# Optimization experiments

Measured on AMD Instinct MI355X. Metric: run time of the kernel, lower is better.

The kernel has to match this reference:

```python
import jax, jax.numpy as jnp
import numpy as np

B, N_HEADS, F_TOK = 8, 12, 768
GRID_H, GRID_W = 32, 32
N_TOK = 1 + GRID_H * GRID_W  # 1025 (readout token + patches)
F_HEAD = F_TOK // N_HEADS    # 64
NUM_DIST = (2 * GRID_H - 1) * (2 * GRID_W - 1) + 3  # 3972


def _build_relpos_index(gh, gw):
    # BEiT-style relative position index with 3 extra slots for the readout token
    coords = np.stack(np.meshgrid(np.arange(gh), np.arange(gw), indexing='ij'))  # (2, gh, gw)
    flat = coords.reshape(2, -1)                                                 # (2, gh*gw)
    rel = flat[:, :, None] - flat[:, None, :]                                    # (2, P, P)
    rel = rel.transpose(1, 2, 0).astype(np.int64)                                # (P, P, 2)
    rel[:, :, 0] += gh - 1
    rel[:, :, 1] += gw - 1
    rel[:, :, 0] *= 2 * gw - 1
    rpi = rel.sum(-1)                                                            # (P, P)
    n = 1 + gh * gw
    nd = (2 * gh - 1) * (2 * gw - 1) + 3
    idx = np.zeros((n, n), dtype=np.int32)
    idx[1:, 1:] = rpi
    idx[0, :] = nd - 3  # readout -> all
    idx[:, 0] = nd - 2  # all -> readout
    idx[0, 0] = nd - 1  # readout -> readout
    return idx


def setup_inputs() -> dict:
    key = jax.random.key(0)
    ks = jax.random.split(key, 7)
    tokens = jax.random.normal(ks[0], (B, N_TOK, F_TOK), dtype=jnp.float32)
    qkv_w = jax.random.normal(ks[1], (3 * F_TOK, F_TOK), dtype=jnp.float32) * 0.02
    q_bias = jax.random.normal(ks[2], (1, N_HEADS, 1, F_HEAD), dtype=jnp.float32) * 0.02
    v_bias = jax.random.normal(ks[3], (1, N_HEADS, 1, F_HEAD), dtype=jnp.float32) * 0.02
    relpos_table = jax.random.normal(ks[4], (NUM_DIST, N_HEADS), dtype=jnp.float32) * 0.02
    proj_w = jax.random.normal(ks[5], (F_TOK, F_TOK), dtype=jnp.float32) * 0.02
    proj_b = jax.random.normal(ks[6], (F_TOK,), dtype=jnp.float32) * 0.02
    relpos_index = jnp.asarray(_build_relpos_index(GRID_H, GRID_W))  # (N, N) int32
    return {
        'tokens': tokens, 'qkv_w': qkv_w, 'q_bias': q_bias, 'v_bias': v_bias,
        'relpos_table': relpos_table, 'proj_w': proj_w, 'proj_b': proj_b,
        'relpos_index': relpos_index, 'patch_h': GRID_H, 'patch_w': GRID_W,
    }


def reference(tokens, qkv_w, q_bias, v_bias, relpos_table, proj_w, proj_b,
              relpos_index, patch_h, patch_w):
    b, n, f_tok = tokens.shape
    # qkv projection (no bias): (B, N, 3F) -> (3, B, H, N, f)
    qkv = tokens @ qkv_w.T
    qkv = qkv.reshape(b, n, 3, N_HEADS, F_HEAD).transpose(2, 0, 3, 1, 4)
    q, k, v = qkv[0], qkv[1], qkv[2]
    q = (q + q_bias) * (F_HEAD ** -0.5)
    v = v + v_bias
    # attention scores: (B, H, N, N)
    attn = jnp.einsum('bhnf,bhmf->bhnm', q, k)
    # relative position bias gather: (N, N, H) -> (H, N, N)
    bias = relpos_table[relpos_index].transpose(2, 0, 1)
    attn = attn + bias[None]
    w = jax.nn.softmax(attn, axis=-1)
    out = jnp.einsum('bhnm,bhmf->bhnf', w, v)
    out = out.transpose(0, 2, 1, 3).reshape(b, n, N_HEADS * F_HEAD)
    return out @ proj_w.T + proj_b
```

## Files before the change

kernel.cpp:

```cpp
#include <hip/hip_runtime.h>

#define B_ 8
#define NH 12
#define NTOK 1025
#define FT 768
#define MROWS (B_*NTOK)
#define NPAD2 1088
#define CH2 34
#define NQT 36
#define NTT 34
#define NRT18 18
#define LOG2E 1.44269504089f

typedef __bf16 bf16x8 __attribute__((ext_vector_type(8)));
typedef __bf16 bf16x2 __attribute__((ext_vector_type(2)));
typedef float floatx4 __attribute__((ext_vector_type(4)));
typedef float floatx16 __attribute__((ext_vector_type(16)));
typedef int intx4 __attribute__((ext_vector_type(4)));

__device__ __forceinline__ void async_ld16(const void* gp, void* lp) {
  __builtin_amdgcn_global_load_lds(
      (const __attribute__((address_space(1))) void*)gp,
      (__attribute__((address_space(3))) void*)lp, 16, 0, 0);
}

__global__ __launch_bounds__(256) void cvt_bf16(const float* __restrict__ src,
                                                __bf16* __restrict__ dst, int n4) {
  int i = blockIdx.x * 256 + threadIdx.x;
  if (i >= n4) return;
  float4 v = ((const float4*)src)[i];
  __bf16 o[4] = {(__bf16)v.x, (__bf16)v.y, (__bf16)v.z, (__bf16)v.w};
  *(uint2*)(dst + 4 * (size_t)i) = *(uint2*)o;
}

__global__ __launch_bounds__(256) void bias_gather_t(
    const int* __restrict__ idx, const float* __restrict__ table,
    __bf16* __restrict__ Bb) {
  const int qt = blockIdx.x, tt = blockIdx.y;
  const int t = threadIdx.x;
  const int lane = t & 63, w = t >> 6;
  const int l31 = lane & 31, hb = lane >> 5;
  int qrow = qt * 32 + l31; if (qrow > NTOK - 1) qrow = NTOK - 1;
  int ids[16]; bool ok[16];
#pragma unroll
  for (int j = 0; j < 16; ++j) {
    const int token = tt * 32 + (j & 3) + 8 * (j >> 2) + 4 * hb;
    ok[j] = token < NTOK;
    ids[j] = ok[j] ? idx[qrow * NTOK + token] : 0;
  }
#pragma unroll
  for (int g = 0; g < 3; ++g) {
    const int h = w + g * 4;
    __bf16 v[16];
#pragma unroll
    for (int j = 0; j < 16; ++j)
      v[j] = ok[j] ? (__bf16)(table[ids[j] * NH + h] * LOG2E) : (__bf16)(-1e30f);
    uint4* dst = (uint4*)(Bb + (((size_t)h * NQT + qt) * NTT + tt) * 1024 + lane * 16);
    dst[0] = ((uint4*)v)[0];
    dst[1] = ((uint4*)v)[1];
  }
}

__device__ __forceinline__ void gemm128_pipe(
    const __bf16* __restrict__ A, const __bf16* __restrict__ W,
    int m0, int n0, int M, __bf16* At, __bf16* Bt, floatx4 acc[4][4]) {
  const int tid = threadIdx.x, wave = tid >> 6, lane = tid & 63;
  const int l = lane & 15, qd = lane >> 4;
  const int wr = wave >> 1, wc = wave & 1;
  const int srow = lane >> 2, sg = lane & 3;
  const int r0 = wave * 32 + srow, r1 = r0 + 16;
  int gm0 = m0 + r0; if (gm0 >= M) gm0 = M - 1;
  int gm1 = m0 + r1; if (gm1 >= M) gm1 = M - 1;
  const int sw0 = (sg ^ (r0 & 3)) * 8;
  const __bf16* gA0 = A + (size_t)gm0 * FT + sw0;
  const __bf16* gA1 = A + (size_t)gm1 * FT + sw0;
  const __bf16* gB0 = W + (size_t)(n0 + r0) * FT + sw0;
  const __bf16* gB1 = W + (size_t)(n0 + r1) * FT + sw0;
  const int woff = wave * 32 * 32;
  const int fsw = (qd ^ (l & 3)) * 8;

  auto issue = [&](int k, int buf) {
    __bf16* a = At + buf * 4096 + woff;
    __bf16* b = Bt + buf * 4096 + woff;
    async_ld16(gA0 + k * 32, a);
    async_ld16(gA1 + k * 32, a + 512);
    async_ld16(gB0 + k * 32, b);
    async_ld16(gB1 + k * 32, b + 512);
  };
  auto step = [&](int buf) {
    __builtin_amdgcn_s_barrier();
    const __bf16* ab = At + buf * 4096;
    const __bf16* bb = Bt + buf * 4096;
    bf16x8 aF[4], bF[4];
#pragma unroll
    for (int t = 0; t < 4; ++t)
      aF[t] = *(const bf16x8*)(ab + (wr * 64 + t * 16 + l) * 32 + fsw);
#pragma unroll
    for (int u = 0; u < 4; ++u)
      bF[u] = *(const bf16x8*)(bb + (wc * 64 + u * 16 + l) * 32 + fsw);
#pragma unroll
    for (int t = 0; t < 4; ++t)
#pragma unroll
      for (int u = 0; u < 4; ++u)
        acc[t][u] = __builtin_amdgcn_mfma_f32_16x16x32_bf16(aF[t], bF[u], acc[t][u], 0, 0, 0);
  };

  issue(0, 0);
  int bk = 0;
  for (int k = 0; k < 23; ++k) {
    int bn = bk + 1; if (bn == 3) bn = 0;
    issue(k + 1, bn);
    __builtin_amdgcn_s_waitcnt(0x0F74);
    step(bk);
    bk = bn;
  }
  __builtin_amdgcn_s_waitcnt(0x0F70);
  step(bk);
}

__global__ __launch_bounds__(256) void qkv_gemm128(
    const __bf16* __restrict__ tokens, const __bf16* __restrict__ qkvw,
    const float* __restrict__ qbias, const float* __restrict__ vbias,
    __bf16* __restrict__ Qb, __bf16* __restrict__ Kc, __bf16* __restrict__ Vc) {
  __shared__ __bf16 At[3 * 4096], Bt[3 * 4096];
  const int u0 = blockIdx.x;
  const int c = u0 & 7, q0 = u0 >> 3;
  const int mi = (q0 / 18) * 8 + c, ni = q0 % 18;
  if (mi >= 65) return;
  const int m0 = mi * 128, n0 = ni * 128;
  const int tid = threadIdx.x, wave = tid >> 6, lane = tid & 63;
  const int l = lane & 15, qd = lane >> 4;
  const int wr = wave >> 1, wc = wave & 1;
  floatx4 acc[4][4];
#pragma unroll
  for (int t = 0; t < 4; ++t)
#pragma unroll
    for (int u = 0; u < 4; ++u) acc[t][u] = (floatx4){0.f, 0.f, 0.f, 0.f};
  gemm128_pipe(tokens, qkvw, m0, n0, MROWS, At, Bt, acc);

  const int which = (n0 / FT);
  const int nrem0 = n0 - which * FT;
#pragma unroll
  for (int u = 0; u < 4; ++u) {
    const int rem = nrem0 + wc * 64 + u * 16 + l;
    const int h = rem >> 6, f = rem & 63;
    const float qb = (which == 0) ? qbias[h * 64 + f] : 0.f;
    const float vb = (which == 2) ? vbias[h * 64 + f] : 0.f;
#pragma unroll
    for (int t = 0; t < 4; ++t) {
#pragma unroll
      for (int r = 0; r < 4; ++r) {
        const int gm = m0 + wr * 64 + t * 16 + qd * 4 + r;
        if (gm >= MROWS) continue;
        const int b = gm / NTOK;
        const int tok = gm - b * NTOK;
        const size_t bh = (size_t)(b * NH + h);
        float v = acc[t][u][r];
        if (which == 0) {
          Qb[(bh * NPAD2 + tok) * 64 + f] = (__bf16)((v + qb) * (0.125f * LOG2E));
        } else if (which == 1) {
          const size_t e = ((size_t)(bh * CH2 + (tok >> 5))) * 2048 +
                           (((f >> 3) * 32 + (tok & 31)) << 3) + (f & 7);
          Kc[e] = (__bf16)v;
        } else {
          const size_t e = ((size_t)(bh * CH2 + (tok >> 5))) * 2048 +
                           (((((tok >> 3) & 3) * 64 + f)) << 3) + (tok & 7);
          Vc[e] = (__bf16)(v + vb);
        }
      }
    }
  }
}

__global__ __launch_bounds__(256) void proj_gemm128(
    const __bf16* __restrict__ Ao, const __bf16* __restrict__ projw,
    const float* __restrict__ projb, float* __restrict__ out) {
  __shared__ __bf16 At[3 * 4096], Bt[3 * 4096];
  const int u0 = blockIdx.x;
  const int c = u0 & 7, q0 = u0 >> 3;
  const int mi = (q0 / 6) * 8 + c, ni = q0 % 6;
  if (mi >= 65) return;
  const int m0 = mi * 128, n0 = ni * 128;
  const int tid = threadIdx.x, wave = tid >> 6, lane = tid & 63;
  const int l = lane & 15, qd = lane >> 4;
  const int wr = wave >> 1, wc = wave & 1;
  floatx4 acc[4][4];
#pragma unroll
  for (int t = 0; t < 4; ++t)
#pragma unroll
    for (int u = 0; u < 4; ++u) acc[t][u] = (floatx4){0.f, 0.f, 0.f, 0.f};
  gemm128_pipe(Ao, projw, m0, n0, MROWS, At, Bt, acc);
#pragma unroll
  for (int u = 0; u < 4; ++u) {
    const int gn = n0 + wc * 64 + u * 16 + l;
    const float pb = projb[gn];
#pragma unroll
    for (int t = 0; t < 4; ++t)
#pragma unroll
      for (int r = 0; r < 4; ++r) {
        const int gm = m0 + wr * 64 + t * 16 + qd * 4 + r;
        if (gm < MROWS) out[(size_t)gm * FT + gn] = acc[t][u][r] + pb;
      }
  }
}

__global__ __launch_bounds__(128) void attn_flash(
    const __bf16* __restrict__ Qb, const __bf16* __restrict__ Kc,
    const __bf16* __restrict__ Vc, const __bf16* __restrict__ Bb,
    __bf16* __restrict__ Ao) {
  __shared__ __bf16 Kl[3][2048], Vl[3][2048];
  const int bh = blockIdx.x;
  const int rt = blockIdx.y;
  const int h = bh % NH, b = bh / NH;
  const int wave = threadIdx.x >> 6, lane = threadIdx.x & 63;
  const int l31 = lane & 31, hb = lane >> 5;
  const int qt = rt * 2 + wave;
  int qrow = qt * 32 + l31; if (qrow > NTOK - 1) qrow = NTOK - 1;

  bf16x8 qf[4];
  {
    const __bf16* Qp = Qb + ((size_t)bh * NPAD2 + qrow) * 64 + hb * 8;
#pragma unroll
    for (int d = 0; d < 4; ++d) qf[d] = *(const bf16x8*)(Qp + d * 16);
  }

  floatx16 o0, o1;
#pragma unroll
  for (int j = 0; j < 16; ++j) { o0[j] = 0.f; o1[j] = 0.f; }
  float lsum = 0.f;

  const __bf16* KVg = (wave ? Vc : Kc) + (size_t)bh * CH2 * 2048;
  const __bf16* Bg = Bb + ((size_t)h * NQT + qt) * NTT * 1024 + lane * 16;

  auto issue = [&](int c, int buf) {
    const __bf16* src = KVg + (size_t)c * 2048 + lane * 8;
    __bf16* dst = wave ? Vl[buf] : Kl[buf];
#pragma unroll
    for (int ii = 0; ii < 4; ++ii) async_ld16(src + ii * 512, dst + ii * 512);
  };

  issue(0, 0);
  bf16x8 bc0 = *(const bf16x8*)(Bg);
  bf16x8 bc1 = *(const bf16x8*)(Bg + 8);
  int buf = 0;
  for (int c = 0; c < CH2; ++c) {
    int nbuf = buf + 1; if (nbuf == 3) nbuf = 0;
    bf16x8 bn0 = bc0, bn1 = bc1;
    if (c + 1 < CH2) {
      issue(c + 1, nbuf);
      bn0 = *(const bf16x8*)(Bg + (size_t)(c + 1) * 1024);
      bn1 = *(const bf16x8*)(Bg + (size_t)(c + 1) * 1024 + 8);
      __builtin_amdgcn_s_waitcnt(0x0F76);
    } else {
      __builtin_amdgcn_s_waitcnt(0x0F70);
    }
    __builtin_amdgcn_s_barrier();

    floatx16 st;
#pragma unroll
    for (int j = 0; j < 16; ++j) st[j] = 0.f;
#pragma unroll
    for (int dk = 0; dk < 4; ++dk) {
      bf16x8 a = *(const bf16x8*)(Kl[buf] + ((dk * 2 + hb) * 32 + l31) * 8);
      st = __builtin_amdgcn_mfma_f32_32x32x16_bf16(a, qf[dk], st, 0, 0, 0);
    }
    float e[16];
#pragma unroll
    for (int j = 0; j < 16; ++j) {
      const float bj = (float)(j < 8 ? bc0[j] : bc1[j - 8]);
      e[j] = __builtin_amdgcn_exp2f(st[j] + bj);
      lsum += e[j];
    }
    int pk[8];
#pragma unroll
    for (int j2 = 0; j2 < 8; ++j2) {
      bf16x2 pr = {(__bf16)e[2 * j2], (__bf16)e[2 * j2 + 1]};
      pk[j2] = __builtin_bit_cast(int, pr);
    }
#pragma unroll
    for (int ks = 0; ks < 2; ++ks) {
      const int r01a = pk[4 * ks + 0], r01b = pk[4 * ks + 1];
      const int r23a = pk[4 * ks + 2], r23b = pk[4 * ks + 3];
      const int t01a = __shfl_xor(r01a, 32), t01b = __shfl_xor(r01b, 32);
      const int t23a = __shfl_xor(r23a, 32), t23b = __shfl_xor(r23b, 32);
      intx4 fi;
      fi[0] = hb ? t23a : r01a;
      fi[1] = hb ? t23b : r01b;
      fi[2] = hb ? r23a : t01a;
      fi[3] = hb ? r23b : t01b;
      bf16x8 pb = __builtin_bit_cast(bf16x8, fi);
      bf16x8 va0 = *(const bf16x8*)(Vl[buf] + ((ks * 2 + hb) * 64 + l31) * 8);
      bf16x8 va1 = *(const bf16x8*)(Vl[buf] + ((ks * 2 + hb) * 64 + 32 + l31) * 8);
      o0 = __builtin_amdgcn_mfma_f32_32x32x16_bf16(va0, pb, o0, 0, 0, 0);
      o1 = __builtin_amdgcn_mfma_f32_32x32x16_bf16(va1, pb, o1, 0, 0, 0);
    }
    bc0 = bn0; bc1 = bn1;
    buf = nbuf;
  }

  const float ltot = lsum + __shfl_xor(lsum, 32);
  const float rinv = 1.0f / ltot;
  const int tok = rt * 64 + wave * 32 + l31;
  if (tok < NTOK) {
    __bf16* op = Ao + ((size_t)b * NTOK + tok) * FT + h * 64;
#pragma unroll
    for (int ft = 0; ft < 2; ++ft) {
#pragma unroll
      for (int jg = 0; jg < 4; ++jg) {
        const int f = ft * 32 + jg * 8 + hb * 4;
        __bf16 v4[4];
#pragma unroll
        for (int q = 0; q < 4; ++q) {
          const float ov = ft ? o1[jg * 4 + q] : o0[jg * 4 + q];
          v4[q] = (__bf16)(ov * rinv);
        }
        *(uint2*)(op + f) = *(uint2*)v4;
      }
    }
  }
}

extern "C" void kernel_launch(void* const* d_in, const int* in_sizes, int n_in,
                              void* d_out, int out_size, void* d_ws, size_t ws_size,
                              hipStream_t stream) {
  (void)in_sizes; (void)n_in; (void)out_size; (void)ws_size;
  const float* tokens = (const float*)d_in[0];
  const float* qkvw   = (const float*)d_in[1];
  const float* qbias  = (const float*)d_in[2];
  const float* vbias  = (const float*)d_in[3];
  const float* table  = (const float*)d_in[4];
  const float* projw  = (const float*)d_in[5];
  const float* projb  = (const float*)d_in[6];
  const int*   rpidx  = (const int*)d_in[7];
  float* out = (float*)d_out;
  char* ws = (char*)d_ws;

  const size_t QB2 = (size_t)B_ * NH * NPAD2 * 64 * 2;
  const size_t BBT = (size_t)NH * NQT * NTT * 1024 * 2;
  const size_t AOB = (size_t)MROWS * FT * 2;
  const size_t WQB = (size_t)3 * FT * FT * 2;
  __bf16* Qb = (__bf16*)(ws);
  __bf16* Kc = (__bf16*)(ws + QB2);
  __bf16* Vc = (__bf16*)(ws + 2 * QB2);
  __bf16* Bb = (__bf16*)(ws + 3 * QB2);
  __bf16* Tb = (__bf16*)(ws + 3 * QB2 + BBT);
  __bf16* Ao = Tb;
  __bf16* Wq = (__bf16*)(ws + 3 * QB2 + BBT + AOB);
  __bf16* Wp = (__bf16*)(ws + 3 * QB2 + BBT + AOB + WQB);

  cvt_bf16<<<(MROWS * FT / 4 + 255) / 256, 256, 0, stream>>>(tokens, Tb, MROWS * FT / 4);
  cvt_bf16<<<(3 * FT * FT / 4 + 255) / 256, 256, 0, stream>>>(qkvw, Wq, 3 * FT * FT / 4);
  cvt_bf16<<<(FT * FT / 4 + 255) / 256, 256, 0, stream>>>(projw, Wp, FT * FT / 4);
  bias_gather_t<<<dim3(NQT, NTT), 256, 0, stream>>>(rpidx, table, Bb);
  qkv_gemm128<<<8 * 9 * 18, 256, 0, stream>>>(Tb, Wq, qbias, vbias, Qb, Kc, Vc);
  attn_flash<<<dim3(B_ * NH, NRT18), 128, 0, stream>>>(Qb, Kc, Vc, Bb, Ao);
  proj_gemm128<<<8 * 9 * 6, 256, 0, stream>>>(Ao, Wp, projb, out);
}
```

Baseline: 272.8 us.

## Deepen load pipelines, tile GEMMs per batch, and pre-transpose the relpos table

Moves the GEMM and attention K/V async-load rings from 3 to 4 buffers with prefetch distance 2, and prefetches bias two chunks ahead. GEMM M-tiles are now aligned per batch (9 tiles of 128 rows per batch), so epilogues take a fast path with hoisted index math and vectorized V stores, and boundary checks only run on the last tile. The relpos table is transposed and pre-scaled to bf16 by a new small kernel, and the bias gather stages indices through shared memory for coalesced reads. Q padding shrinks to 1025 rows. The gains come at the cost of more LDS per block and one extra launch.

```diff
diff --git a/kernel.cpp b/kernel.cpp
--- a/kernel.cpp
+++ b/kernel.cpp
@@ -5,11 +5,12 @@
 #define NTOK 1025
 #define FT 768
 #define MROWS (B_*NTOK)
-#define NPAD2 1088
+#define QPAD 1025
 #define CH2 34
 #define NQT 36
 #define NTT 34
 #define NRT18 18
+#define NDIST 3972
 #define LOG2E 1.44269504089f
 
 typedef __bf16 bf16x8 __attribute__((ext_vector_type(8)));
@@ -33,28 +34,48 @@
   *(uint2*)(dst + 4 * (size_t)i) = *(uint2*)o;
 }
 
+__global__ __launch_bounds__(256) void table_prep(const float* __restrict__ table,
+                                                  __bf16* __restrict__ tableT) {
+  int i = blockIdx.x * 256 + threadIdx.x;
+  if (i >= NH * NDIST) return;
+  int h = i / NDIST, d = i - h * NDIST;
+  tableT[i] = (__bf16)(table[(size_t)d * NH + h] * LOG2E);
+}
+
 __global__ __launch_bounds__(256) void bias_gather_t(
-    const int* __restrict__ idx, const float* __restrict__ table,
+    const int* __restrict__ idx, const __bf16* __restrict__ tableT,
     __bf16* __restrict__ Bb) {
+  __shared__ int ids_l[32][33];
   const int qt = blockIdx.x, tt = blockIdx.y;
   const int t = threadIdx.x;
+  {
+    const int row = t >> 3, c4 = (t & 7) * 4;
+    int qrow = qt * 32 + row; if (qrow > NTOK - 1) qrow = NTOK - 1;
+    const int* src = idx + (size_t)qrow * NTOK;
+#pragma unroll
+    for (int j = 0; j < 4; ++j) {
+      int token = tt * 32 + c4 + j; if (token > NTOK - 1) token = NTOK - 1;
+      ids_l[row][c4 + j] = src[token];
+    }
+  }
+  __syncthreads();
   const int lane = t & 63, w = t >> 6;
   const int l31 = lane & 31, hb = lane >> 5;
-  int qrow = qt * 32 + l31; if (qrow > NTOK - 1) qrow = NTOK - 1;
   int ids[16]; bool ok[16];
 #pragma unroll
   for (int j = 0; j < 16; ++j) {
-    const int token = tt * 32 + (j & 3) + 8 * (j >> 2) + 4 * hb;
-    ok[j] = token < NTOK;
-    ids[j] = ok[j] ? idx[qrow * NTOK + token] : 0;
+    const int col = (j & 3) + 8 * (j >> 2) + 4 * hb;
+    ok[j] = tt * 32 + col < NTOK;
+    ids[j] = ids_l[l31][col];
   }
 #pragma unroll
   for (int g = 0; g < 3; ++g) {
     const int h = w + g * 4;
-    __bf16 v[16];
+    const __bf16* tb = tableT + (size_t)h * NDIST;
+    __bf16 v[16] __attribute__((aligned(16)));
 #pragma unroll
     for (int j = 0; j < 16; ++j)
-      v[j] = ok[j] ? (__bf16)(table[ids[j] * NH + h] * LOG2E) : (__bf16)(-1e30f);
+      v[j] = ok[j] ? tb[ids[j]] : (__bf16)(-1e30f);
     uint4* dst = (uint4*)(Bb + (((size_t)h * NQT + qt) * NTT + tt) * 1024 + lane * 16);
     dst[0] = ((uint4*)v)[0];
     dst[1] = ((uint4*)v)[1];
@@ -63,14 +84,14 @@
 
 __device__ __forceinline__ void gemm128_pipe(
     const __bf16* __restrict__ A, const __bf16* __restrict__ W,
-    int m0, int n0, int M, __bf16* At, __bf16* Bt, floatx4 acc[4][4]) {
+    int am0, int n0, int amax, __bf16* At, __bf16* Bt, floatx4 acc[4][4]) {
   const int tid = threadIdx.x, wave = tid >> 6, lane = tid & 63;
   const int l = lane & 15, qd = lane >> 4;
   const int wr = wave >> 1, wc = wave & 1;
   const int srow = lane >> 2, sg = lane & 3;
   const int r0 = wave * 32 + srow, r1 = r0 + 16;
-  int gm0 = m0 + r0; if (gm0 >= M) gm0 = M - 1;
-  int gm1 = m0 + r1; if (gm1 >= M) gm1 = M - 1;
+  int gm0 = am0 + r0; if (gm0 > amax) gm0 = amax;
+  int gm1 = am0 + r1; if (gm1 > amax) gm1 = amax;
   const int sw0 = (sg ^ (r0 & 3)) * 8;
   const __bf16* gA0 = A + (size_t)gm0 * FT + sw0;
   const __bf16* gA1 = A + (size_t)gm1 * FT + sw0;
@@ -106,28 +127,31 @@
   };
 
   issue(0, 0);
-  int bk = 0;
-  for (int k = 0; k < 23; ++k) {
-    int bn = bk + 1; if (bn == 3) bn = 0;
-    issue(k + 1, bn);
-    __builtin_amdgcn_s_waitcnt(0x0F74);
-    step(bk);
-    bk = bn;
-  }
-  __builtin_amdgcn_s_waitcnt(0x0F70);
-  step(bk);
+  issue(1, 1);
+  for (int k = 0; k < 24; ++k) {
+    if (k + 2 < 24) {
+      issue(k + 2, (k + 2) & 3);
+      __builtin_amdgcn_s_waitcnt(0x0F78);
+    } else if (k + 1 < 24) {
+      __builtin_amdgcn_s_waitcnt(0x0F74);
+    } else {
+      __builtin_amdgcn_s_waitcnt(0x0F70);
+    }
+    step(k & 3);
+  }
 }
 
 __global__ __launch_bounds__(256) void qkv_gemm128(
     const __bf16* __restrict__ tokens, const __bf16* __restrict__ qkvw,
     const float* __restrict__ qbias, const float* __restrict__ vbias,
     __bf16* __restrict__ Qb, __bf16* __restrict__ Kc, __bf16* __restrict__ Vc) {
-  __shared__ __bf16 At[3 * 4096], Bt[3 * 4096];
+  __shared__ __bf16 At[4 * 4096], Bt[4 * 4096];
   const int u0 = blockIdx.x;
   const int c = u0 & 7, q0 = u0 >> 3;
-  const int mi = (q0 / 18) * 8 + c, ni = q0 % 18;
-  if (mi >= 65) return;
-  const int m0 = mi * 128, n0 = ni * 128;
+  const int mt = (q0 / 18) * 8 + c, ni = q0 % 18;
+  const int b = mt / 9, ml = mt - b * 9;
+  const int am0 = b * NTOK + ml * 128, amax = b * NTOK + 1024;
+  const int n0 = ni * 128;
   const int tid = threadIdx.x, wave = tid >> 6, lane = tid & 63;
   const int l = lane & 15, qd = lane >> 4;
   const int wr = wave >> 1, wc = wave & 1;
@@ -136,36 +160,86 @@
   for (int t = 0; t < 4; ++t)
 #pragma unroll
     for (int u = 0; u < 4; ++u) acc[t][u] = (floatx4){0.f, 0.f, 0.f, 0.f};
-  gemm128_pipe(tokens, qkvw, m0, n0, MROWS, At, Bt, acc);
-
-  const int which = (n0 / FT);
-  const int nrem0 = n0 - which * FT;
-#pragma unroll
-  for (int u = 0; u < 4; ++u) {
-    const int rem = nrem0 + wc * 64 + u * 16 + l;
-    const int h = rem >> 6, f = rem & 63;
-    const float qb = (which == 0) ? qbias[h * 64 + f] : 0.f;
-    const float vb = (which == 2) ? vbias[h * 64 + f] : 0.f;
-#pragma unroll
-    for (int t = 0; t < 4; ++t) {
-#pragma unroll
-      for (int r = 0; r < 4; ++r) {
-        const int gm = m0 + wr * 64 + t * 16 + qd * 4 + r;
-        if (gm >= MROWS) continue;
-        const int b = gm / NTOK;
-        const int tok = gm - b * NTOK;
-        const size_t bh = (size_t)(b * NH + h);
-        float v = acc[t][u][r];
-        if (which == 0) {
-          Qb[(bh * NPAD2 + tok) * 64 + f] = (__bf16)((v + qb) * (0.125f * LOG2E));
-        } else if (which == 1) {
-          const size_t e = ((size_t)(bh * CH2 + (tok >> 5))) * 2048 +
-                           (((f >> 3) * 32 + (tok & 31)) << 3) + (f & 7);
-          Kc[e] = (__bf16)v;
+  gemm128_pipe(tokens, qkvw, am0, n0, amax, At, Bt, acc);
+
+  const int which = ni / 6;
+  const int nrem0 = (ni - which * 6) * 128;
+  const bool full = (ml < 8);
+  const int tokb = ml * 128 + wr * 64 + qd * 4;
+
+  if (which == 0) {
+#pragma unroll
+    for (int u = 0; u < 4; ++u) {
+      const int rem = nrem0 + wc * 64 + u * 16 + l;
+      const int h = rem >> 6, f = rem & 63;
+      const size_t bhq = ((size_t)(b * NH + h)) * QPAD;
+      const float qb = qbias[h * 64 + f];
+#pragma unroll
+      for (int t = 0; t < 4; ++t) {
+        const int tok = tokb + t * 16;
+        if (full) {
+          __bf16* qp = Qb + (bhq + tok) * 64 + f;
+#pragma unroll
+          for (int r = 0; r < 4; ++r)
+            qp[r * 64] = (__bf16)((acc[t][u][r] + qb) * (0.125f * LOG2E));
         } else {
-          const size_t e = ((size_t)(bh * CH2 + (tok >> 5))) * 2048 +
-                           (((((tok >> 3) & 3) * 64 + f)) << 3) + (tok & 7);
-          Vc[e] = (__bf16)(v + vb);
+#pragma unroll
+          for (int r = 0; r < 4; ++r)
+            if (tok + r < NTOK)
+              Qb[(bhq + tok + r) * 64 + f] = (__bf16)((acc[t][u][r] + qb) * (0.125f * LOG2E));
+        }
+      }
+    }
+  } else if (which == 1) {
+#pragma unroll
+    for (int u = 0; u < 4; ++u) {
+      const int rem = nrem0 + wc * 64 + u * 16 + l;
+      const int f = rem & 63;
+      const size_t bhc = ((size_t)(b * NH + (rem >> 6))) * CH2;
+      const int dgo = (f >> 3) * 256 + (f & 7);
+#pragma unroll
+      for (int t = 0; t < 4; ++t) {
+        const int tok = tokb + t * 16;
+        if (full) {
+          const size_t base = (bhc + (tok >> 5)) * 2048 + dgo + (tok & 31) * 8;
+#pragma unroll
+          for (int r = 0; r < 4; ++r) Kc[base + r * 8] = (__bf16)acc[t][u][r];
+        } else {
+#pragma unroll
+          for (int r = 0; r < 4; ++r) {
+            const int tk = tok + r;
+            if (tk < NTOK)
+              Kc[(bhc + (tk >> 5)) * 2048 + (f >> 3) * 256 + (tk & 31) * 8 + (f & 7)] =
+                  (__bf16)acc[t][u][r];
+          }
+        }
+      }
+    }
+  } else {
+#pragma unroll
+    for (int u = 0; u < 4; ++u) {
+      const int rem = nrem0 + wc * 64 + u * 16 + l;
+      const int h = rem >> 6, f = rem & 63;
+      const size_t bhc = ((size_t)(b * NH + h)) * CH2;
+      const float vb = vbias[h * 64 + f];
+#pragma unroll
+      for (int t = 0; t < 4; ++t) {
+        const int tok = tokb + t * 16;
+        if (full) {
+          __bf16 v4[4] __attribute__((aligned(8)));
+#pragma unroll
+          for (int r = 0; r < 4; ++r) v4[r] = (__bf16)(acc[t][u][r] + vb);
+          const size_t e = (bhc + (tok >> 5)) * 2048 +
+                           ((((tok >> 3) & 3) * 64 + f) << 3) + (tok & 7);
+          *(uint2*)(Vc + e) = *(const uint2*)v4;
+        } else {
+#pragma unroll
+          for (int r = 0; r < 4; ++r) {
+            const int tk = tok + r;
+            if (tk < NTOK)
+              Vc[(bhc + (tk >> 5)) * 2048 + ((((tk >> 3) & 3) * 64 + f) << 3) + (tk & 7)] =
+                  (__bf16)(acc[t][u][r] + vb);
+          }
         }
       }
     }
@@ -175,12 +249,13 @@
 __global__ __launch_bounds__(256) void proj_gemm128(
     const __bf16* __restrict__ Ao, const __bf16* __restrict__ projw,
     const float* __restrict__ projb, float* __restrict__ out) {
-  __shared__ __bf16 At[3 * 4096], Bt[3 * 4096];
+  __shared__ __bf16 At[4 * 4096], Bt[4 * 4096];
   const int u0 = blockIdx.x;
   const int c = u0 & 7, q0 = u0 >> 3;
-  const int mi = (q0 / 6) * 8 + c, ni = q0 % 6;
-  if (mi >= 65) return;
-  const int m0 = mi * 128, n0 = ni * 128;
+  const int mt = (q0 / 6) * 8 + c, ni = q0 % 6;
+  const int b = mt / 9, ml = mt - b * 9;
+  const int am0 = b * NTOK + ml * 128, amax = b * NTOK + 1024;
+  const int n0 = ni * 128;
   const int tid = threadIdx.x, wave = tid >> 6, lane = tid & 63;
   const int l = lane & 15, qd = lane >> 4;
   const int wr = wave >> 1, wc = wave & 1;
@@ -189,18 +264,28 @@
   for (int t = 0; t < 4; ++t)
 #pragma unroll
     for (int u = 0; u < 4; ++u) acc[t][u] = (floatx4){0.f, 0.f, 0.f, 0.f};
-  gemm128_pipe(Ao, projw, m0, n0, MROWS, At, Bt, acc);
+  gemm128_pipe(Ao, projw, am0, n0, amax, At, Bt, acc);
+
+  const bool full = (ml < 8);
+  const int tokb = ml * 128 + wr * 64 + qd * 4;
+  const size_t rowb = (size_t)b * NTOK;
 #pragma unroll
   for (int u = 0; u < 4; ++u) {
     const int gn = n0 + wc * 64 + u * 16 + l;
     const float pb = projb[gn];
 #pragma unroll
-    for (int t = 0; t < 4; ++t)
-#pragma unroll
-      for (int r = 0; r < 4; ++r) {
-        const int gm = m0 + wr * 64 + t * 16 + qd * 4 + r;
-        if (gm < MROWS) out[(size_t)gm * FT + gn] = acc[t][u][r] + pb;
+    for (int t = 0; t < 4; ++t) {
+      const int tok = tokb + t * 16;
+      if (full) {
+        float* op = out + (rowb + tok) * FT + gn;
+#pragma unroll
+        for (int r = 0; r < 4; ++r) op[(size_t)r * FT] = acc[t][u][r] + pb;
+      } else {
+#pragma unroll
+        for (int r = 0; r < 4; ++r)
+          if (tok + r < NTOK) out[(rowb + tok + r) * FT + gn] = acc[t][u][r] + pb;
       }
+    }
   }
 }
 
@@ -208,7 +293,7 @@
     const __bf16* __restrict__ Qb, const __bf16* __restrict__ Kc,
     const __bf16* __restrict__ Vc, const __bf16* __restrict__ Bb,
     __bf16* __restrict__ Ao) {
-  __shared__ __bf16 Kl[3][2048], Vl[3][2048];
+  __shared__ __bf16 Kl[4][2048], Vl[4][2048];
   const int bh = blockIdx.x;
   const int rt = blockIdx.y;
   const int h = bh % NH, b = bh / NH;
@@ -219,7 +304,7 @@
 
   bf16x8 qf[4];
   {
-    const __bf16* Qp = Qb + ((size_t)bh * NPAD2 + qrow) * 64 + hb * 8;
+    const __bf16* Qp = Qb + ((size_t)bh * QPAD + qrow) * 64 + hb * 8;
 #pragma unroll
     for (int d = 0; d < 4; ++d) qf[d] = *(const bf16x8*)(Qp + d * 16);
   }
@@ -239,29 +324,34 @@
     for (int ii = 0; ii < 4; ++ii) async_ld16(src + ii * 512, dst + ii * 512);
   };
 
-  issue(0, 0);
   bf16x8 bc0 = *(const bf16x8*)(Bg);
   bf16x8 bc1 = *(const bf16x8*)(Bg + 8);
-  int buf = 0;
+  bf16x8 b10 = *(const bf16x8*)(Bg + 1024);
+  bf16x8 b11 = *(const bf16x8*)(Bg + 1024 + 8);
+  issue(0, 0);
+  issue(1, 1);
   for (int c = 0; c < CH2; ++c) {
-    int nbuf = buf + 1; if (nbuf == 3) nbuf = 0;
-    bf16x8 bn0 = bc0, bn1 = bc1;
-    if (c + 1 < CH2) {
-      issue(c + 1, nbuf);
-      bn0 = *(const bf16x8*)(Bg + (size_t)(c + 1) * 1024);
-      bn1 = *(const bf16x8*)(Bg + (size_t)(c + 1) * 1024 + 8);
-      __builtin_amdgcn_s_waitcnt(0x0F76);
+    bf16x8 b20 = b10, b21 = b11;
+    if (c + 2 < CH2) {
+      b20 = *(const bf16x8*)(Bg + (size_t)(c + 2) * 1024);
+      b21 = *(const bf16x8*)(Bg + (size_t)(c + 2) * 1024 + 8);
+      issue(c + 2, (c + 2) & 3);
+      __builtin_amdgcn_s_waitcnt(0x0F7A);
+    } else if (c + 1 < CH2) {
+      __builtin_amdgcn_s_waitcnt(0x0F74);
     } else {
       __builtin_amdgcn_s_waitcnt(0x0F70);
     }
     __builtin_amdgcn_s_barrier();
+    const __bf16* Kb = Kl[c & 3];
+    const __bf16* Vb = Vl[c & 3];
 
     floatx16 st;
 #pragma unroll
     for (int j = 0; j < 16; ++j) st[j] = 0.f;
 #pragma unroll
     for (int dk = 0; dk < 4; ++dk) {
-      bf16x8 a = *(const bf16x8*)(Kl[buf] + ((dk * 2 + hb) * 32 + l31) * 8);
+      bf16x8 a = *(const bf16x8*)(Kb + ((dk * 2 + hb) * 32 + l31) * 8);
       st = __builtin_amdgcn_mfma_f32_32x32x16_bf16(a, qf[dk], st, 0, 0, 0);
     }
     float e[16];
@@ -289,13 +379,12 @@
       fi[2] = hb ? r23a : t01a;
       fi[3] = hb ? r23b : t01b;
       bf16x8 pb = __builtin_bit_cast(bf16x8, fi);
-      bf16x8 va0 = *(const bf16x8*)(Vl[buf] + ((ks * 2 + hb) * 64 + l31) * 8);
-      bf16x8 va1 = *(const bf16x8*)(Vl[buf] + ((ks * 2 + hb) * 64 + 32 + l31) * 8);
+      bf16x8 va0 = *(const bf16x8*)(Vb + ((ks * 2 + hb) * 64 + l31) * 8);
+      bf16x8 va1 = *(const bf16x8*)(Vb + ((ks * 2 + hb) * 64 + 32 + l31) * 8);
       o0 = __builtin_amdgcn_mfma_f32_32x32x16_bf16(va0, pb, o0, 0, 0, 0);
       o1 = __builtin_amdgcn_mfma_f32_32x32x16_bf16(va1, pb, o1, 0, 0, 0);
     }
-    bc0 = bn0; bc1 = bn1;
-    buf = nbuf;
+    bc0 = b10; bc1 = b11; b10 = b20; b11 = b21;
   }
 
   const float ltot = lsum + __shfl_xor(lsum, 32);
@@ -308,7 +397,7 @@
 #pragma unroll
       for (int jg = 0; jg < 4; ++jg) {
         const int f = ft * 32 + jg * 8 + hb * 4;
-        __bf16 v4[4];
+        __bf16 v4[4] __attribute__((aligned(8)));
 #pragma unroll
         for (int q = 0; q < 4; ++q) {
           const float ov = ft ? o1[jg * 4 + q] : o0[jg * 4 + q];
@@ -335,23 +424,27 @@
   float* out = (float*)d_out;
   char* ws = (char*)d_ws;
 
-  const size_t QB2 = (size_t)B_ * NH * NPAD2 * 64 * 2;
+  const size_t QBQ = (size_t)B_ * NH * QPAD * 64 * 2;
+  const size_t KVB = (size_t)B_ * NH * CH2 * 2048 * 2;
   const size_t BBT = (size_t)NH * NQT * NTT * 1024 * 2;
   const size_t AOB = (size_t)MROWS * FT * 2;
   const size_t WQB = (size_t)3 * FT * FT * 2;
+  const size_t WPB = (size_t)FT * FT * 2;
   __bf16* Qb = (__bf16*)(ws);
-  __bf16* Kc = (__bf16*)(ws + QB2);
-  __bf16* Vc = (__bf16*)(ws + 2 * QB2);
-  __bf16* Bb = (__bf16*)(ws + 3 * QB2);
-  __bf16* Tb = (__bf16*)(ws + 3 * QB2 + BBT);
+  __bf16* Kc = (__bf16*)(ws + QBQ);
+  __bf16* Vc = (__bf16*)(ws + QBQ + KVB);
+  __bf16* Bb = (__bf16*)(ws + QBQ + 2 * KVB);
+  __bf16* Tb = (__bf16*)(ws + QBQ + 2 * KVB + BBT);
   __bf16* Ao = Tb;
-  __bf16* Wq = (__bf16*)(ws + 3 * QB2 + BBT + AOB);
-  __bf16* Wp = (__bf16*)(ws + 3 * QB2 + BBT + AOB + WQB);
+  __bf16* Wq = (__bf16*)(ws + QBQ + 2 * KVB + BBT + AOB);
+  __bf16* Wp = (__bf16*)(ws + QBQ + 2 * KVB + BBT + AOB + WQB);
+  __bf16* Tt = (__bf16*)(ws + QBQ + 2 * KVB + BBT + AOB + WQB + WPB);
 
   cvt_bf16<<<(MROWS * FT / 4 + 255) / 256, 256, 0, stream>>>(tokens, Tb, MROWS * FT / 4);
   cvt_bf16<<<(3 * FT * FT / 4 + 255) / 256, 256, 0, stream>>>(qkvw, Wq, 3 * FT * FT / 4);
   cvt_bf16<<<(FT * FT / 4 + 255) / 256, 256, 0, stream>>>(projw, Wp, FT * FT / 4);
-  bias_gather_t<<<dim3(NQT, NTT), 256, 0, stream>>>(rpidx, table, Bb);
+  table_prep<<<(NH * NDIST + 255) / 256, 256, 0, stream>>>(table, Tt);
+  bias_gather_t<<<dim3(NQT, NTT), 256, 0, stream>>>(rpidx, Tt, Bb);
   qkv_gemm128<<<8 * 9 * 18, 256, 0, stream>>>(Tb, Wq, qbias, vbias, Qb, Kc, Vc);
   attn_flash<<<dim3(B_ * NH, NRT18), 128, 0, stream>>>(Qb, Kc, Vc, Bb, Ao);
   proj_gemm128<<<8 * 9 * 6, 256, 0, stream>>>(Ao, Wp, projb, out);
```

Measured after the change: 261.6 us. 4.1% less time.
